# Performance work log

Measured on AMD Instinct MI355X. Metric: run time of the kernel, lower is better.

The kernel has to match this reference:

```python
import jax, jax.numpy as jnp
import numpy as np

TOP_K = 2
NEG_INF = float('-inf')


def setup_inputs() -> dict:
    key = jax.random.key(0)
    kx, kw = jax.random.split(key)
    B, S, D, E = 4, 4096, 2048, 64
    x = jax.random.normal(kx, (B, S, D), dtype=jnp.float32)
    W = jax.random.normal(kw, (E, D), dtype=jnp.float32) * (1.0 / np.sqrt(D))
    b = jnp.zeros((E,), dtype=jnp.float32)
    return {"x": x, "W": W, "b": b}


def reference(x, W, b):
    # logits: [B, S, E] -- small linear gate
    logits = jnp.einsum('bsd,ed->bse', x, W) + b
    B, S, E = logits.shape
    # top-k over experts
    topk_vals, topk_idx = jax.lax.top_k(logits, TOP_K)  # [B,S,K]
    # scatter top-k logits into a -inf filled tensor
    flat_vals = topk_vals.reshape(-1, TOP_K)            # [T, K]
    flat_idx = topk_idx.reshape(-1, TOP_K)              # [T, K]
    T = flat_idx.shape[0]
    sparse = jnp.full((T, E), NEG_INF, dtype=logits.dtype)
    sparse = sparse.at[jnp.arange(T)[:, None], flat_idx].set(flat_vals)
    # softmax over experts; -inf entries become exactly 0
    router_output = jax.nn.softmax(sparse, axis=-1).reshape(B, S, E)
    return router_output, topk_idx
```

## Files before the change

kernel.cpp:

```cpp
#include <hip/hip_runtime.h>
#include <math.h>


#define RD 2048
#define RE 64
#define TB 16
#define NCH 32

typedef __attribute__((ext_vector_type(8))) short bf16x8;
typedef __attribute__((ext_vector_type(4))) float f32x4;
typedef __attribute__((ext_vector_type(4))) unsigned int u32x4;
typedef __attribute__((ext_vector_type(2))) unsigned int u32x2;

__device__ __forceinline__ unsigned short f2b(float f) {
    unsigned int u = __float_as_uint(f);
    unsigned int r = ((u >> 16) & 1u) + 0x7fffu;
    return (unsigned short)((u + r) >> 16);
}
__device__ __forceinline__ float b2f(unsigned short h) {
    return __uint_as_float(((unsigned int)h) << 16);
}

__device__ __forceinline__ int swz(int f) {
    return (f << 2) ^ (((f >> 3) & 7) << 2);
}

__device__ __forceinline__ void cvt8(const f32x4 a, const f32x4 bq,
                                     unsigned int* h, unsigned int* l,
                                     unsigned int* l2) {
    float v[8] = {a.x, a.y, a.z, a.w, bq.x, bq.y, bq.z, bq.w};
#pragma unroll
    for (int j = 0; j < 4; ++j) {
        const float a0 = v[2 * j], a1 = v[2 * j + 1];
        const unsigned short h0 = f2b(a0); const float r0 = a0 - b2f(h0);
        const unsigned short h1 = f2b(a1); const float r1 = a1 - b2f(h1);
        const unsigned short m0 = f2b(r0); const float s0 = r0 - b2f(m0);
        const unsigned short m1 = f2b(r1); const float s1 = r1 - b2f(m1);
        const unsigned short q0 = f2b(s0);
        const unsigned short q1 = f2b(s1);
        h[j]  = (unsigned int)h0 | ((unsigned int)h1 << 16);
        l[j]  = (unsigned int)m0 | ((unsigned int)m1 << 16);
        l2[j] = (unsigned int)q0 | ((unsigned int)q1 << 16);
    }
}

__device__ __forceinline__ void cvt4(const f32x4 a,
                                     unsigned int* h, unsigned int* l,
                                     unsigned int* l2) {
    float v[4] = {a.x, a.y, a.z, a.w};
#pragma unroll
    for (int j = 0; j < 2; ++j) {
        const float a0 = v[2 * j], a1 = v[2 * j + 1];
        const unsigned short h0 = f2b(a0); const float r0 = a0 - b2f(h0);
        const unsigned short h1 = f2b(a1); const float r1 = a1 - b2f(h1);
        const unsigned short m0 = f2b(r0); const float s0 = r0 - b2f(m0);
        const unsigned short m1 = f2b(r1); const float s1 = r1 - b2f(m1);
        const unsigned short q0 = f2b(s0);
        const unsigned short q1 = f2b(s1);
        h[j]  = (unsigned int)h0 | ((unsigned int)h1 << 16);
        l[j]  = (unsigned int)m0 | ((unsigned int)m1 << 16);
        l2[j] = (unsigned int)q0 | ((unsigned int)q1 << 16);
    }
}

__global__ __launch_bounds__(256) void wprep_kernel(
    const float* __restrict__ W, unsigned int* __restrict__ WB)
{
    const int ks = blockIdx.x;
    const int et = threadIdx.x >> 6;
    const int lane = threadIdx.x & 63;
    const int e = et * 16 + (lane & 15);
    const int k0 = ks * 32 + (lane >> 4) * 8;
    const float* src = W + (size_t)e * RD + k0;
    const f32x4 a = *(const f32x4*)(src);
    const f32x4 bq = *(const f32x4*)(src + 4);
    unsigned int h[4], l[4], l2[4];
    cvt8(a, bq, h, l, l2);
    unsigned int* dst = WB + (size_t)((ks * 4 + et) * 3) * 256 + lane * 4;
    *(u32x4*)(dst)       = *(u32x4*)h;
    *(u32x4*)(dst + 256) = *(u32x4*)l;
    *(u32x4*)(dst + 512) = *(u32x4*)l2;
}

__global__ __launch_bounds__(256, 4) void topk_router_kernel(
    const float* __restrict__ x,
    const unsigned int* __restrict__ WB,
    const float* __restrict__ b,
    float* __restrict__ out_router,
    float* __restrict__ out_idx,
    int total_tokens)
{
    const int tid = threadIdx.x;
    const int lane = tid & 63;
    const int et = __builtin_amdgcn_readfirstlane(tid >> 6);
    const int tok0 = blockIdx.x * TB;

    __shared__ __align__(16) unsigned int SM[2][2][3][256];

    const int stok = tid >> 4;
    const int part = tid & 15;
    const int tmax = total_tokens - 1;
    const float* gsrc = x + (size_t)min(tok0 + stok, tmax) * RD + part * 4;
    const int s_ks = part >> 3;
    const int s_f  = ((part >> 1) & 3) * 16 + stok;
    const int s_off = swz(s_f) + (part & 1) * 2;

    f32x4 acc = {0.f, 0.f, 0.f, 0.f};
    double acc64[4] = {0.0, 0.0, 0.0, 0.0};

    {
        const f32x4 v0 = *(const f32x4*)(gsrc);
        unsigned int h[2], l[2], l2[2];
        cvt4(v0, h, l, l2);
        *(u32x2*)&SM[0][s_ks][0][s_off] = *(u32x2*)h;
        *(u32x2*)&SM[0][s_ks][1][s_off] = *(u32x2*)l;
        *(u32x2*)&SM[0][s_ks][2][s_off] = *(u32x2*)l2;
    }
    f32x4 pf = *(const f32x4*)(gsrc + 64);
    __syncthreads();

#pragma unroll 1
    for (int c = 0; c < NCH; ++c) {
        const int buf = c & 1;
        const int cn = (c + 2 < NCH) ? (c + 2) : 0;
        const f32x4 nx = *(const f32x4*)(gsrc + (size_t)cn * 64);

#pragma unroll
        for (int ks = 0; ks < 2; ++ks) {
            const bf16x8 Ah  = *(const bf16x8*)&SM[buf][ks][0][swz(lane)];
            const bf16x8 Al  = *(const bf16x8*)&SM[buf][ks][1][swz(lane)];
            const bf16x8 Al2 = *(const bf16x8*)&SM[buf][ks][2][swz(lane)];
            const int ksg = c * 2 + ks;
            const unsigned int* wp =
                WB + (size_t)((ksg * 4 + et) * 3) * 256 + lane * 4;
            const bf16x8 Bh  = *(const bf16x8*)(wp);
            const bf16x8 Bl  = *(const bf16x8*)(wp + 256);
            const bf16x8 Bl2 = *(const bf16x8*)(wp + 512);
            acc = __builtin_amdgcn_mfma_f32_16x16x32_bf16(Ah,  Bh,  acc, 0, 0, 0);
            acc = __builtin_amdgcn_mfma_f32_16x16x32_bf16(Ah,  Bl,  acc, 0, 0, 0);
            acc = __builtin_amdgcn_mfma_f32_16x16x32_bf16(Al,  Bh,  acc, 0, 0, 0);
            acc = __builtin_amdgcn_mfma_f32_16x16x32_bf16(Al,  Bl,  acc, 0, 0, 0);
            acc = __builtin_amdgcn_mfma_f32_16x16x32_bf16(Ah,  Bl2, acc, 0, 0, 0);
            acc = __builtin_amdgcn_mfma_f32_16x16x32_bf16(Al2, Bh,  acc, 0, 0, 0);
        }

        if ((c & 7) == 7) {
            acc64[0] += (double)acc.x; acc64[1] += (double)acc.y;
            acc64[2] += (double)acc.z; acc64[3] += (double)acc.w;
            acc = (f32x4){0.f, 0.f, 0.f, 0.f};
        }

        if (c + 1 < NCH) {
            unsigned int h[2], l[2], l2[2];
            cvt4(pf, h, l, l2);
            const int nbuf = (c + 1) & 1;
            *(u32x2*)&SM[nbuf][s_ks][0][s_off] = *(u32x2*)h;
            *(u32x2*)&SM[nbuf][s_ks][1][s_off] = *(u32x2*)l;
            *(u32x2*)&SM[nbuf][s_ks][2][s_off] = *(u32x2*)l2;
        }
        pf = nx;
        __syncthreads();
    }

    double* lg = (double*)&SM[0][0][0][0];
#pragma unroll
    for (int r = 0; r < 4; ++r) {
        const int t = (lane >> 4) * 4 + r;
        const int e = et * 16 + (lane & 15);
        lg[(size_t)t * 66 + e] = acc64[r];
    }
    __syncthreads();

    const double bias = (double)b[lane];

#pragma unroll 1
    for (int i = 0; i < 4; ++i) {
        const int t = et * 4 + i;
        const int token = tok0 + t;
        const double v = lg[(size_t)t * 66 + lane] + bias;

        double bestv = v;
        int besti = lane;
#pragma unroll
        for (int off = 32; off > 0; off >>= 1) {
            double ov = __shfl_xor(bestv, off, 64);
            int oi = __shfl_xor(besti, off, 64);
            if (ov > bestv || (ov == bestv && oi < besti)) { bestv = ov; besti = oi; }
        }

        double v2 = (lane == besti) ? -INFINITY : v;
        double best2v = v2;
        int best2i = lane;
#pragma unroll
        for (int off = 32; off > 0; off >>= 1) {
            double ov = __shfl_xor(best2v, off, 64);
            int oi = __shfl_xor(best2i, off, 64);
            if (ov > best2v || (ov == best2v && oi < best2i)) { best2v = ov; best2i = oi; }
        }

        const float e2 = expf((float)(best2v - bestv));
        const float denom = 1.0f + e2;
        const float p1v = 1.0f / denom;
        const float p2v = e2 / denom;

        if (token < total_tokens) {
            float outv = 0.0f;
            if (lane == besti) outv = p1v;
            else if (lane == best2i) outv = p2v;
            out_router[(size_t)token * RE + lane] = outv;
            if (lane == 0) {
                out_idx[(size_t)token * 2 + 0] = (float)besti;
                out_idx[(size_t)token * 2 + 1] = (float)best2i;
            }
        }
    }
}

extern "C" void kernel_launch(void* const* d_in, const int* in_sizes, int n_in,
                              void* d_out, int out_size, void* d_ws, size_t ws_size,
                              hipStream_t stream) {
    const float* x = (const float*)d_in[0];
    const float* W = (const float*)d_in[1];
    const float* b = (const float*)d_in[2];

    const int E = in_sizes[2];
    const int D = in_sizes[1] / E;
    const int T = in_sizes[0] / D;
    (void)E; (void)D;

    unsigned int* WB = (unsigned int*)d_ws;
    float* out_router = (float*)d_out;
    float* out_idx = out_router + (size_t)T * RE;

    wprep_kernel<<<64, 256, 0, stream>>>(W, WB);

    const int grid = (T + TB - 1) / TB;
    topk_router_kernel<<<grid, 256, 0, stream>>>(x, WB, b, out_router, out_idx, T);
}
```

Measured before the change: 54.17 us.

## Split K across waves with register-direct A fragments instead of shared-memory staging

Each of the four waves now takes a quarter of the D dimension for all 16 tokens and all 64 experts, keeping four accumulators. A fragments are loaded straight from global memory into registers and converted there, which removes the shared-memory staging, the swizzle and the per-chunk __syncthreads. Partial sums from the four waves are combined through shared memory at the end. In exchange, the periodic fp64 accumulation is dropped in favour of plain fp32 accumulators, which may cost some accuracy for top-k tie ordering, and register pressure rises.

```diff
diff --git a/kernel.cpp b/kernel.cpp
--- a/kernel.cpp
+++ b/kernel.cpp
@@ -5,12 +5,11 @@
 #define RD 2048
 #define RE 64
 #define TB 16
-#define NCH 32
+#define NCQ 8
 
 typedef __attribute__((ext_vector_type(8))) short bf16x8;
 typedef __attribute__((ext_vector_type(4))) float f32x4;
 typedef __attribute__((ext_vector_type(4))) unsigned int u32x4;
-typedef __attribute__((ext_vector_type(2))) unsigned int u32x2;
 
 __device__ __forceinline__ unsigned short f2b(float f) {
     unsigned int u = __float_as_uint(f);
@@ -21,35 +20,12 @@
     return __uint_as_float(((unsigned int)h) << 16);
 }
 
-__device__ __forceinline__ int swz(int f) {
-    return (f << 2) ^ (((f >> 3) & 7) << 2);
-}
-
 __device__ __forceinline__ void cvt8(const f32x4 a, const f32x4 bq,
                                      unsigned int* h, unsigned int* l,
                                      unsigned int* l2) {
     float v[8] = {a.x, a.y, a.z, a.w, bq.x, bq.y, bq.z, bq.w};
 #pragma unroll
     for (int j = 0; j < 4; ++j) {
-        const float a0 = v[2 * j], a1 = v[2 * j + 1];
-        const unsigned short h0 = f2b(a0); const float r0 = a0 - b2f(h0);
-        const unsigned short h1 = f2b(a1); const float r1 = a1 - b2f(h1);
-        const unsigned short m0 = f2b(r0); const float s0 = r0 - b2f(m0);
-        const unsigned short m1 = f2b(r1); const float s1 = r1 - b2f(m1);
-        const unsigned short q0 = f2b(s0);
-        const unsigned short q1 = f2b(s1);
-        h[j]  = (unsigned int)h0 | ((unsigned int)h1 << 16);
-        l[j]  = (unsigned int)m0 | ((unsigned int)m1 << 16);
-        l2[j] = (unsigned int)q0 | ((unsigned int)q1 << 16);
-    }
-}
-
-__device__ __forceinline__ void cvt4(const f32x4 a,
-                                     unsigned int* h, unsigned int* l,
-                                     unsigned int* l2) {
-    float v[4] = {a.x, a.y, a.z, a.w};
-#pragma unroll
-    for (int j = 0; j < 2; ++j) {
         const float a0 = v[2 * j], a1 = v[2 * j + 1];
         const unsigned short h0 = f2b(a0); const float r0 = a0 - b2f(h0);
         const unsigned short h1 = f2b(a1); const float r1 = a1 - b2f(h1);
@@ -82,6 +58,18 @@
     *(u32x4*)(dst + 512) = *(u32x4*)l2;
 }
 
+#define SIXMFMA(AH, AL, AQ, ACC, WP) do {                                  \
+    const bf16x8 Bh_ = *(const bf16x8*)(WP);                               \
+    const bf16x8 Bl_ = *(const bf16x8*)((WP) + 256);                       \
+    const bf16x8 Bq_ = *(const bf16x8*)((WP) + 512);                       \
+    ACC = __builtin_amdgcn_mfma_f32_16x16x32_bf16(AH, Bh_, ACC, 0, 0, 0);  \
+    ACC = __builtin_amdgcn_mfma_f32_16x16x32_bf16(AH, Bl_, ACC, 0, 0, 0);  \
+    ACC = __builtin_amdgcn_mfma_f32_16x16x32_bf16(AL, Bh_, ACC, 0, 0, 0);  \
+    ACC = __builtin_amdgcn_mfma_f32_16x16x32_bf16(AL, Bl_, ACC, 0, 0, 0);  \
+    ACC = __builtin_amdgcn_mfma_f32_16x16x32_bf16(AH, Bq_, ACC, 0, 0, 0);  \
+    ACC = __builtin_amdgcn_mfma_f32_16x16x32_bf16(AQ, Bh_, ACC, 0, 0, 0);  \
+} while (0)
+
 __global__ __launch_bounds__(256, 4) void topk_router_kernel(
     const float* __restrict__ x,
     const unsigned int* __restrict__ WB,
@@ -92,82 +80,74 @@
 {
     const int tid = threadIdx.x;
     const int lane = tid & 63;
-    const int et = __builtin_amdgcn_readfirstlane(tid >> 6);
+    const int wq = __builtin_amdgcn_readfirstlane(tid >> 6);
     const int tok0 = blockIdx.x * TB;
 
-    __shared__ __align__(16) unsigned int SM[2][2][3][256];
-
-    const int stok = tid >> 4;
-    const int part = tid & 15;
+    __shared__ __align__(16) float PS[4][TB][68];
+
     const int tmax = total_tokens - 1;
-    const float* gsrc = x + (size_t)min(tok0 + stok, tmax) * RD + part * 4;
-    const int s_ks = part >> 3;
-    const int s_f  = ((part >> 1) & 3) * 16 + stok;
-    const int s_off = swz(s_f) + (part & 1) * 2;
-
-    f32x4 acc = {0.f, 0.f, 0.f, 0.f};
-    double acc64[4] = {0.0, 0.0, 0.0, 0.0};
-
-    {
-        const f32x4 v0 = *(const f32x4*)(gsrc);
-        unsigned int h[2], l[2], l2[2];
-        cvt4(v0, h, l, l2);
-        *(u32x2*)&SM[0][s_ks][0][s_off] = *(u32x2*)h;
-        *(u32x2*)&SM[0][s_ks][1][s_off] = *(u32x2*)l;
-        *(u32x2*)&SM[0][s_ks][2][s_off] = *(u32x2*)l2;
-    }
-    f32x4 pf = *(const f32x4*)(gsrc + 64);
-    __syncthreads();
+    const int row = min(tok0 + (lane & 15), tmax);
+    const float* ga = x + (size_t)row * RD + wq * (RD / 4) + (lane >> 4) * 8;
+
+    f32x4 acc0 = {0.f, 0.f, 0.f, 0.f};
+    f32x4 acc1 = {0.f, 0.f, 0.f, 0.f};
+    f32x4 acc2 = {0.f, 0.f, 0.f, 0.f};
+    f32x4 acc3 = {0.f, 0.f, 0.f, 0.f};
+
+    f32x4 p0 = *(const f32x4*)(ga + 0);
+    f32x4 p1 = *(const f32x4*)(ga + 4);
+    f32x4 p2 = *(const f32x4*)(ga + 32);
+    f32x4 p3 = *(const f32x4*)(ga + 36);
 
 #pragma unroll 1
-    for (int c = 0; c < NCH; ++c) {
-        const int buf = c & 1;
-        const int cn = (c + 2 < NCH) ? (c + 2) : 0;
-        const f32x4 nx = *(const f32x4*)(gsrc + (size_t)cn * 64);
-
-#pragma unroll
-        for (int ks = 0; ks < 2; ++ks) {
-            const bf16x8 Ah  = *(const bf16x8*)&SM[buf][ks][0][swz(lane)];
-            const bf16x8 Al  = *(const bf16x8*)&SM[buf][ks][1][swz(lane)];
-            const bf16x8 Al2 = *(const bf16x8*)&SM[buf][ks][2][swz(lane)];
-            const int ksg = c * 2 + ks;
-            const unsigned int* wp =
-                WB + (size_t)((ksg * 4 + et) * 3) * 256 + lane * 4;
-            const bf16x8 Bh  = *(const bf16x8*)(wp);
-            const bf16x8 Bl  = *(const bf16x8*)(wp + 256);
-            const bf16x8 Bl2 = *(const bf16x8*)(wp + 512);
-            acc = __builtin_amdgcn_mfma_f32_16x16x32_bf16(Ah,  Bh,  acc, 0, 0, 0);
-            acc = __builtin_amdgcn_mfma_f32_16x16x32_bf16(Ah,  Bl,  acc, 0, 0, 0);
-            acc = __builtin_amdgcn_mfma_f32_16x16x32_bf16(Al,  Bh,  acc, 0, 0, 0);
-            acc = __builtin_amdgcn_mfma_f32_16x16x32_bf16(Al,  Bl,  acc, 0, 0, 0);
-            acc = __builtin_amdgcn_mfma_f32_16x16x32_bf16(Ah,  Bl2, acc, 0, 0, 0);
-            acc = __builtin_amdgcn_mfma_f32_16x16x32_bf16(Al2, Bh,  acc, 0, 0, 0);
-        }
-
-        if ((c & 7) == 7) {
-            acc64[0] += (double)acc.x; acc64[1] += (double)acc.y;
-            acc64[2] += (double)acc.z; acc64[3] += (double)acc.w;
-            acc = (f32x4){0.f, 0.f, 0.f, 0.f};
-        }
-
-        if (c + 1 < NCH) {
-            unsigned int h[2], l[2], l2[2];
-            cvt4(pf, h, l, l2);
-            const int nbuf = (c + 1) & 1;
-            *(u32x2*)&SM[nbuf][s_ks][0][s_off] = *(u32x2*)h;
-            *(u32x2*)&SM[nbuf][s_ks][1][s_off] = *(u32x2*)l;
-            *(u32x2*)&SM[nbuf][s_ks][2][s_off] = *(u32x2*)l2;
-        }
-        pf = nx;
-        __syncthreads();
-    }
-
-    double* lg = (double*)&SM[0][0][0][0];
+    for (int c = 0; c < NCQ; ++c) {
+        const int cn = (c + 1 < NCQ) ? (c + 1) : 0;
+        const float* gn = ga + (size_t)cn * 64;
+        const f32x4 n0 = *(const f32x4*)(gn + 0);
+        const f32x4 n1 = *(const f32x4*)(gn + 4);
+        const f32x4 n2 = *(const f32x4*)(gn + 32);
+        const f32x4 n3 = *(const f32x4*)(gn + 36);
+
+        unsigned int h0[4], l0[4], q0[4], h1[4], l1[4], q1[4];
+        cvt8(p0, p1, h0, l0, q0);
+        cvt8(p2, p3, h1, l1, q1);
+        const bf16x8 A0h = *(const bf16x8*)h0;
+        const bf16x8 A0l = *(const bf16x8*)l0;
+        const bf16x8 A0q = *(const bf16x8*)q0;
+        const bf16x8 A1h = *(const bf16x8*)h1;
+        const bf16x8 A1l = *(const bf16x8*)l1;
+        const bf16x8 A1q = *(const bf16x8*)q1;
+
+        const int ksg0 = wq * 16 + c * 2;
+        const unsigned int* wp00 = WB + (size_t)((ksg0 * 4 + 0) * 3) * 256 + lane * 4;
+        const unsigned int* wp01 = WB + (size_t)((ksg0 * 4 + 1) * 3) * 256 + lane * 4;
+        const unsigned int* wp02 = WB + (size_t)((ksg0 * 4 + 2) * 3) * 256 + lane * 4;
+        const unsigned int* wp03 = WB + (size_t)((ksg0 * 4 + 3) * 3) * 256 + lane * 4;
+        SIXMFMA(A0h, A0l, A0q, acc0, wp00);
+        SIXMFMA(A0h, A0l, A0q, acc1, wp01);
+        SIXMFMA(A0h, A0l, A0q, acc2, wp02);
+        SIXMFMA(A0h, A0l, A0q, acc3, wp03);
+
+        const int ksg1 = ksg0 + 1;
+        const unsigned int* wp10 = WB + (size_t)((ksg1 * 4 + 0) * 3) * 256 + lane * 4;
+        const unsigned int* wp11 = WB + (size_t)((ksg1 * 4 + 1) * 3) * 256 + lane * 4;
+        const unsigned int* wp12 = WB + (size_t)((ksg1 * 4 + 2) * 3) * 256 + lane * 4;
+        const unsigned int* wp13 = WB + (size_t)((ksg1 * 4 + 3) * 3) * 256 + lane * 4;
+        SIXMFMA(A1h, A1l, A1q, acc0, wp10);
+        SIXMFMA(A1h, A1l, A1q, acc1, wp11);
+        SIXMFMA(A1h, A1l, A1q, acc2, wp12);
+        SIXMFMA(A1h, A1l, A1q, acc3, wp13);
+
+        p0 = n0; p1 = n1; p2 = n2; p3 = n3;
+    }
+
 #pragma unroll
     for (int r = 0; r < 4; ++r) {
         const int t = (lane >> 4) * 4 + r;
-        const int e = et * 16 + (lane & 15);
-        lg[(size_t)t * 66 + e] = acc64[r];
+        PS[wq][t][0 * 16 + (lane & 15)] = acc0[r];
+        PS[wq][t][1 * 16 + (lane & 15)] = acc1[r];
+        PS[wq][t][2 * 16 + (lane & 15)] = acc2[r];
+        PS[wq][t][3 * 16 + (lane & 15)] = acc3[r];
     }
     __syncthreads();
 
@@ -175,9 +155,10 @@
 
 #pragma unroll 1
     for (int i = 0; i < 4; ++i) {
-        const int t = et * 4 + i;
+        const int t = wq * 4 + i;
         const int token = tok0 + t;
-        const double v = lg[(size_t)t * 66 + lane] + bias;
+        const double v = (double)PS[0][t][lane] + (double)PS[1][t][lane]
+                       + (double)PS[2][t][lane] + (double)PS[3][t][lane] + bias;
 
         double bestv = v;
         int besti = lane;
```

Measured after the change: 59.33 us. +9.5%, slower.

## Stage larger 256-wide K chunks per iteration with single LDS buffer and XOR swizzle

Applied to the files above, without the earlier changes.

Restructures the main loop from 32 chunks of 64 K-elements to 8 chunks of 256. Each wave loads four token rows per chunk with a one-chunk register prefetch, converts them to three bf16 splits, and writes them into a single LDS buffer laid out per k-step with an XOR swizzle. Each chunk then runs 8 k-steps of MFMA between two barriers. This cuts loop and barrier count per K and widens the global loads, but drops LDS double buffering, so conversion and MFMA no longer overlap across chunks. The fp64 flush cadence is adjusted to keep the same K span per flush.

```diff
diff --git a/kernel.cpp b/kernel.cpp
--- a/kernel.cpp
+++ b/kernel.cpp
@@ -5,7 +5,7 @@
 #define RD 2048
 #define RE 64
 #define TB 16
-#define NCH 32
+#define NCH 8
 
 typedef __attribute__((ext_vector_type(8))) short bf16x8;
 typedef __attribute__((ext_vector_type(4))) float f32x4;
@@ -19,10 +19,6 @@
 }
 __device__ __forceinline__ float b2f(unsigned short h) {
     return __uint_as_float(((unsigned int)h) << 16);
-}
-
-__device__ __forceinline__ int swz(int f) {
-    return (f << 2) ^ (((f >> 3) & 7) << 2);
 }
 
 __device__ __forceinline__ void cvt8(const f32x4 a, const f32x4 bq,
@@ -95,74 +91,92 @@
     const int et = __builtin_amdgcn_readfirstlane(tid >> 6);
     const int tok0 = blockIdx.x * TB;
 
-    __shared__ __align__(16) unsigned int SM[2][2][3][256];
-
-    const int stok = tid >> 4;
-    const int part = tid & 15;
+    __shared__ __align__(16) unsigned int FR[8][3][64][4];
+
     const int tmax = total_tokens - 1;
-    const float* gsrc = x + (size_t)min(tok0 + stok, tmax) * RD + part * 4;
-    const int s_ks = part >> 3;
-    const int s_f  = ((part >> 1) & 3) * 16 + stok;
-    const int s_off = swz(s_f) + (part & 1) * 2;
+    const float* g0 = x + (size_t)min(tok0 + 0 + et, tmax) * RD + lane * 4;
+    const float* g1 = x + (size_t)min(tok0 + 4 + et, tmax) * RD + lane * 4;
+    const float* g2 = x + (size_t)min(tok0 + 8 + et, tmax) * RD + lane * 4;
+    const float* g3 = x + (size_t)min(tok0 + 12 + et, tmax) * RD + lane * 4;
+
+    const int w_ks = lane >> 3;
+    const int w_kg = (lane >> 1) & 3;
+    const int w_d0 = (lane & 1) * 2;
 
     f32x4 acc = {0.f, 0.f, 0.f, 0.f};
     double acc64[4] = {0.0, 0.0, 0.0, 0.0};
 
-    {
-        const f32x4 v0 = *(const f32x4*)(gsrc);
-        unsigned int h[2], l[2], l2[2];
-        cvt4(v0, h, l, l2);
-        *(u32x2*)&SM[0][s_ks][0][s_off] = *(u32x2*)h;
-        *(u32x2*)&SM[0][s_ks][1][s_off] = *(u32x2*)l;
-        *(u32x2*)&SM[0][s_ks][2][s_off] = *(u32x2*)l2;
-    }
-    f32x4 pf = *(const f32x4*)(gsrc + 64);
-    __syncthreads();
+    f32x4 c0 = *(const f32x4*)(g0);
+    f32x4 c1 = *(const f32x4*)(g1);
+    f32x4 c2 = *(const f32x4*)(g2);
+    f32x4 c3 = *(const f32x4*)(g3);
 
 #pragma unroll 1
     for (int c = 0; c < NCH; ++c) {
-        const int buf = c & 1;
-        const int cn = (c + 2 < NCH) ? (c + 2) : 0;
-        const f32x4 nx = *(const f32x4*)(gsrc + (size_t)cn * 64);
-
-#pragma unroll
-        for (int ks = 0; ks < 2; ++ks) {
-            const bf16x8 Ah  = *(const bf16x8*)&SM[buf][ks][0][swz(lane)];
-            const bf16x8 Al  = *(const bf16x8*)&SM[buf][ks][1][swz(lane)];
-            const bf16x8 Al2 = *(const bf16x8*)&SM[buf][ks][2][swz(lane)];
-            const int ksg = c * 2 + ks;
+        const int cn = (c + 1 < NCH) ? (c + 1) : 0;
+        const f32x4 n0 = *(const f32x4*)(g0 + (size_t)cn * 256);
+        const f32x4 n1 = *(const f32x4*)(g1 + (size_t)cn * 256);
+        const f32x4 n2 = *(const f32x4*)(g2 + (size_t)cn * 256);
+        const f32x4 n3 = *(const f32x4*)(g3 + (size_t)cn * 256);
+
+        __syncthreads();
+
+        {
+            unsigned int h_[2], l_[2], q_[2];
+            int fl_;
+            cvt4(c0, h_, l_, q_);
+            fl_ = (w_kg * 16 + 0 + et) ^ w_ks;
+            *(u32x2*)&FR[w_ks][0][fl_][w_d0] = *(u32x2*)h_;
+            *(u32x2*)&FR[w_ks][1][fl_][w_d0] = *(u32x2*)l_;
+            *(u32x2*)&FR[w_ks][2][fl_][w_d0] = *(u32x2*)q_;
+            cvt4(c1, h_, l_, q_);
+            fl_ = (w_kg * 16 + 4 + et) ^ w_ks;
+            *(u32x2*)&FR[w_ks][0][fl_][w_d0] = *(u32x2*)h_;
+            *(u32x2*)&FR[w_ks][1][fl_][w_d0] = *(u32x2*)l_;
+            *(u32x2*)&FR[w_ks][2][fl_][w_d0] = *(u32x2*)q_;
+            cvt4(c2, h_, l_, q_);
+            fl_ = (w_kg * 16 + 8 + et) ^ w_ks;
+            *(u32x2*)&FR[w_ks][0][fl_][w_d0] = *(u32x2*)h_;
+            *(u32x2*)&FR[w_ks][1][fl_][w_d0] = *(u32x2*)l_;
+            *(u32x2*)&FR[w_ks][2][fl_][w_d0] = *(u32x2*)q_;
+            cvt4(c3, h_, l_, q_);
+            fl_ = (w_kg * 16 + 12 + et) ^ w_ks;
+            *(u32x2*)&FR[w_ks][0][fl_][w_d0] = *(u32x2*)h_;
+            *(u32x2*)&FR[w_ks][1][fl_][w_d0] = *(u32x2*)l_;
+            *(u32x2*)&FR[w_ks][2][fl_][w_d0] = *(u32x2*)q_;
+        }
+        __syncthreads();
+
+#pragma unroll
+        for (int ks = 0; ks < 8; ++ks) {
+            const bf16x8 Ah = *(const bf16x8*)&FR[ks][0][lane ^ ks][0];
+            const bf16x8 Al = *(const bf16x8*)&FR[ks][1][lane ^ ks][0];
+            const bf16x8 Aq = *(const bf16x8*)&FR[ks][2][lane ^ ks][0];
+            const int ksg = c * 8 + ks;
             const unsigned int* wp =
                 WB + (size_t)((ksg * 4 + et) * 3) * 256 + lane * 4;
-            const bf16x8 Bh  = *(const bf16x8*)(wp);
-            const bf16x8 Bl  = *(const bf16x8*)(wp + 256);
-            const bf16x8 Bl2 = *(const bf16x8*)(wp + 512);
-            acc = __builtin_amdgcn_mfma_f32_16x16x32_bf16(Ah,  Bh,  acc, 0, 0, 0);
-            acc = __builtin_amdgcn_mfma_f32_16x16x32_bf16(Ah,  Bl,  acc, 0, 0, 0);
-            acc = __builtin_amdgcn_mfma_f32_16x16x32_bf16(Al,  Bh,  acc, 0, 0, 0);
-            acc = __builtin_amdgcn_mfma_f32_16x16x32_bf16(Al,  Bl,  acc, 0, 0, 0);
-            acc = __builtin_amdgcn_mfma_f32_16x16x32_bf16(Ah,  Bl2, acc, 0, 0, 0);
-            acc = __builtin_amdgcn_mfma_f32_16x16x32_bf16(Al2, Bh,  acc, 0, 0, 0);
-        }
-
-        if ((c & 7) == 7) {
+            const bf16x8 Bh = *(const bf16x8*)(wp);
+            const bf16x8 Bl = *(const bf16x8*)(wp + 256);
+            const bf16x8 Bq = *(const bf16x8*)(wp + 512);
+            acc = __builtin_amdgcn_mfma_f32_16x16x32_bf16(Ah, Bh, acc, 0, 0, 0);
+            acc = __builtin_amdgcn_mfma_f32_16x16x32_bf16(Ah, Bl, acc, 0, 0, 0);
+            acc = __builtin_amdgcn_mfma_f32_16x16x32_bf16(Al, Bh, acc, 0, 0, 0);
+            acc = __builtin_amdgcn_mfma_f32_16x16x32_bf16(Al, Bl, acc, 0, 0, 0);
+            acc = __builtin_amdgcn_mfma_f32_16x16x32_bf16(Ah, Bq, acc, 0, 0, 0);
+            acc = __builtin_amdgcn_mfma_f32_16x16x32_bf16(Aq, Bh, acc, 0, 0, 0);
+        }
+
+        if ((c & 1) == 1) {
             acc64[0] += (double)acc.x; acc64[1] += (double)acc.y;
             acc64[2] += (double)acc.z; acc64[3] += (double)acc.w;
             acc = (f32x4){0.f, 0.f, 0.f, 0.f};
         }
 
-        if (c + 1 < NCH) {
-            unsigned int h[2], l[2], l2[2];
-            cvt4(pf, h, l, l2);
-            const int nbuf = (c + 1) & 1;
-            *(u32x2*)&SM[nbuf][s_ks][0][s_off] = *(u32x2*)h;
-            *(u32x2*)&SM[nbuf][s_ks][1][s_off] = *(u32x2*)l;
-            *(u32x2*)&SM[nbuf][s_ks][2][s_off] = *(u32x2*)l2;
-        }
-        pf = nx;
-        __syncthreads();
-    }
-
-    double* lg = (double*)&SM[0][0][0][0];
+        c0 = n0; c1 = n1; c2 = n2; c3 = n3;
+    }
+
+    __syncthreads();
+    double* lg = (double*)&FR[0][0][0][0];
 #pragma unroll
     for (int r = 0; r < 4; ++r) {
         const int t = (lane >> 4) * 4 + r;
```

New measurement: 58.74 us. 1.08x slower.
